# Performance work log

Hardware: AMD Instinct MI355X
Metric: run time of the kernel (lower is better)

The kernel has to match this reference:

```python
import jax, jax.numpy as jnp
import numpy as np

B, T, E, H = 2, 2048, 1024, 16
D = E // H            # head dim = 64
ROT = D // 2          # rotary_dim = 32 (only first half of head dim is rotated)
THETA = 10000.0


def _rope(x):
    # x: (B, H, T, D). Faithful to rotary_embedding_torch.rotate_queries_or_keys
    # with dim=ROT: rotate first ROT features, interleaved-pair style, pass rest.
    t = x.shape[-2]
    inv = 1.0 / (THETA ** (jnp.arange(0, ROT, 2, dtype=jnp.float32) / ROT))   # (ROT//2,)
    freqs = jnp.arange(t, dtype=jnp.float32)[:, None] * inv[None, :]          # (T, ROT//2)
    freqs = jnp.repeat(freqs, 2, axis=-1)                                      # (T, ROT)
    cos, sin = jnp.cos(freqs), jnp.sin(freqs)
    xr, xp = x[..., :ROT], x[..., ROT:]
    p = xr.reshape(*xr.shape[:-1], ROT // 2, 2)
    rot = jnp.stack((-p[..., 1], p[..., 0]), axis=-1).reshape(xr.shape)
    return jnp.concatenate([xr * cos + rot * sin, xp], axis=-1)


def setup_inputs() -> dict:
    key = jax.random.key(0)
    k1, k2, k3 = jax.random.split(key, 3)
    query = jax.random.normal(k1, (B, T, E), dtype=jnp.float32)
    inputs = {
        "query": query,
        "key": query,            # ignored (cross_attention=False)
        "value": query,          # ignored
        "padding_mask": jnp.ones((B, T), dtype=bool),
        "in_proj_weight": jax.random.uniform(k2, (3 * E, E), dtype=jnp.float32),
        "out_proj_weight": jax.random.normal(k3, (E, E), dtype=jnp.float32) * (E ** -0.5),
    }
    return inputs


def reference(query, key, value, padding_mask, in_proj_weight, out_proj_weight):
    # cross_attention=False: key/value are overwritten by query
    key = query
    value = query
    q = query @ in_proj_weight[:E].T
    k = key @ in_proj_weight[E:2 * E].T
    v = value @ in_proj_weight[2 * E:].T
    # NOTE: raw reshape (B,T,E)->(B,H,T,D), exactly as in the torch module
    q = q.reshape(B, H, T, D)
    k = k.reshape(B, H, T, D)
    v = v.reshape(B, H, T, D)
    q = _rope(q)
    k = _rope(k)   # causal self-attention path: rotate keys too
    causal = jnp.tril(jnp.ones((T, T), dtype=bool))                 # (T, T)
    mask = causal[None, None] & padding_mask[:, None, None, :]      # (B,1,T,T) -> broadcast over H
    scores = jnp.einsum("bhqd,bhkd->bhqk", q, k) / jnp.sqrt(jnp.float32(D))
    scores = jnp.where(mask, scores, -jnp.inf)
    attn = jax.nn.softmax(scores, axis=-1)
    x = jnp.einsum("bhqk,bhkd->bhqd", attn, v)
    x = x.reshape(B, T, E)      # raw reshape back, as in torch
    return x @ out_proj_weight.T
```

## Files before the change

### kernel.cpp

```cpp
#include <hip/hip_runtime.h>
#include <stdint.h>

#define T_ 2048
#define E_ 1024

typedef __attribute__((ext_vector_type(8))) __bf16 bf16x8;
typedef __attribute__((ext_vector_type(4))) float f32x4;

__device__ __forceinline__ void gload_lds16(const void* g, void* l) {
  __builtin_amdgcn_global_load_lds(
      (const __attribute__((address_space(1))) unsigned int*)g,
      (__attribute__((address_space(3))) unsigned int*)l, 16, 0, 0);
}

__global__ __launch_bounds__(256) void k_split(const float4* __restrict__ src,
                                               ushort4* __restrict__ hi,
                                               ushort4* __restrict__ lo, int n4) {
  int i = blockIdx.x * 256 + threadIdx.x;
  if (i >= n4) return;
  float4 x = src[i];
  float xs[4] = {x.x, x.y, x.z, x.w};
  union { __bf16 b[4]; ushort4 u; } H, L;
#pragma unroll
  for (int j = 0; j < 4; ++j) {
    __bf16 h = (__bf16)xs[j];
    H.b[j] = h;
    L.b[j] = (__bf16)(xs[j] - (float)h);
  }
  hi[i] = H.u;
  lo[i] = L.u;
}

__global__ __launch_bounds__(256) void k_cvt(const float4* __restrict__ src,
                                             ushort4* __restrict__ dst, int n4) {
  int i = blockIdx.x * 256 + threadIdx.x;
  if (i >= n4) return;
  float4 x = src[i];
  float xs[4] = {x.x, x.y, x.z, x.w};
  union { __bf16 b[4]; ushort4 u; } H;
#pragma unroll
  for (int j = 0; j < 4; ++j) H.b[j] = (__bf16)xs[j];
  dst[i] = H.u;
}

__global__ __launch_bounds__(256) void k_table(float2* __restrict__ cs) {
  int i = blockIdx.x * 256 + threadIdx.x;
  int t = i >> 4, f = i & 15;
  double inv = pow(10000.0, -(double)f / 16.0);
  double ang = (double)t * inv;
  cs[i] = make_float2((float)cos(ang), (float)sin(ang));
}

template <int EPI, bool HILO>
__global__ __launch_bounds__(256) void k_gemm(const __bf16* __restrict__ Ah,
                                              const __bf16* __restrict__ Al,
                                              const __bf16* __restrict__ Bh,
                                              const __bf16* __restrict__ Bl,
                                              int M, int N, int K,
                                              const float2* __restrict__ cs,
                                              __bf16* __restrict__ qhi,
                                              __bf16* __restrict__ qlo,
                                              __bf16* __restrict__ khi,
                                              __bf16* __restrict__ klo,
                                              __bf16* __restrict__ v16,
                                              float* __restrict__ C32) {
  __shared__ __align__(16) __bf16 AsH[128 * 32];
  __shared__ __align__(16) __bf16 BsH[128 * 32];
  __shared__ __align__(16) __bf16 AsL[HILO ? 128 * 32 : 4];
  __shared__ __align__(16) __bf16 BsL[HILO ? 128 * 32 : 4];
  const int tid = threadIdx.x, lane = tid & 63, w = tid >> 6;
  const int wm = w >> 1, wn = w & 1;
  const int g = lane >> 4, d = lane & 15;
  const int m0 = blockIdx.y * 128, n0 = blockIdx.x * 128;

  f32x4 acc[4][4];
#pragma unroll
  for (int i = 0; i < 4; ++i)
#pragma unroll
    for (int j = 0; j < 4; ++j) acc[i][j] = (f32x4)(0.0f);

  const int row0 = tid >> 2, kc = tid & 3;
  const int row1 = 64 + row0;

  for (int k0 = 0; k0 < K; k0 += 32) {
    __syncthreads();
    gload_lds16(Ah + (size_t)(m0 + row0) * K + k0 + kc * 8, &AsH[w * 512]);
    gload_lds16(Ah + (size_t)(m0 + row1) * K + k0 + kc * 8, &AsH[2048 + w * 512]);
    gload_lds16(Bh + (size_t)(n0 + row0) * K + k0 + kc * 8, &BsH[w * 512]);
    gload_lds16(Bh + (size_t)(n0 + row1) * K + k0 + kc * 8, &BsH[2048 + w * 512]);
    if constexpr (HILO) {
      gload_lds16(Al + (size_t)(m0 + row0) * K + k0 + kc * 8, &AsL[w * 512]);
      gload_lds16(Al + (size_t)(m0 + row1) * K + k0 + kc * 8, &AsL[2048 + w * 512]);
      gload_lds16(Bl + (size_t)(n0 + row0) * K + k0 + kc * 8, &BsL[w * 512]);
      gload_lds16(Bl + (size_t)(n0 + row1) * K + k0 + kc * 8, &BsL[2048 + w * 512]);
    }
    __syncthreads();
    bf16x8 ah[4], bh[4], al[4], bl[4];
#pragma unroll
    for (int i = 0; i < 4; ++i) {
      ah[i] = *(const bf16x8*)&AsH[(wm * 64 + i * 16 + d) * 32 + g * 8];
      bh[i] = *(const bf16x8*)&BsH[(wn * 64 + i * 16 + d) * 32 + g * 8];
      if constexpr (HILO) {
        al[i] = *(const bf16x8*)&AsL[(wm * 64 + i * 16 + d) * 32 + g * 8];
        bl[i] = *(const bf16x8*)&BsL[(wn * 64 + i * 16 + d) * 32 + g * 8];
      }
    }
#pragma unroll
    for (int i = 0; i < 4; ++i)
#pragma unroll
      for (int j = 0; j < 4; ++j) {
        acc[i][j] = __builtin_amdgcn_mfma_f32_16x16x32_bf16(ah[i], bh[j], acc[i][j], 0, 0, 0);
        if constexpr (HILO) {
          acc[i][j] = __builtin_amdgcn_mfma_f32_16x16x32_bf16(al[i], bh[j], acc[i][j], 0, 0, 0);
          acc[i][j] = __builtin_amdgcn_mfma_f32_16x16x32_bf16(ah[i], bl[j], acc[i][j], 0, 0, 0);
        }
      }
  }

#pragma unroll
  for (int i = 0; i < 4; ++i) {
    const int rbase = m0 + wm * 64 + i * 16 + g * 4;
#pragma unroll
    for (int j = 0; j < 4; ++j) {
      const int col = n0 + wn * 64 + j * 16 + d;
#pragma unroll
      for (int r = 0; r < 4; ++r) {
        const float vv = acc[i][j][r];
        const int row = rbase + r;
        if constexpr (EPI == 0) {
          const float xp = __shfl_xor(vv, 1);
          const int which = col >> 10;
          const int cl = col & 1023;
          const int d2 = cl & 63;
          const int t2 = (row & 127) * 16 + (cl >> 6);
          float y;
          if (d2 < 32) {
            const float2 cse = cs[t2 * 16 + (d2 >> 1)];
            y = (d2 & 1) ? (vv * cse.x + xp * cse.y) : (vv * cse.x - xp * cse.y);
          } else {
            y = vv;
          }
          if (which == 0) y *= 0.18033688011112042f;
          const __bf16 hi = (__bf16)y;
          const __bf16 lo = (__bf16)(y - (float)hi);
          const size_t off = (size_t)row * 1024 + cl;
          (which ? khi : qhi)[off] = hi;
          (which ? klo : qlo)[off] = lo;
        } else if constexpr (EPI == 1) {
          C32[(size_t)row * N + col] = vv;
        } else {
          v16[(size_t)row * N + col] = (__bf16)vv;
        }
      }
    }
  }
}

__global__ __launch_bounds__(256) void k_vtrans(const __bf16* __restrict__ v16,
                                                __bf16* __restrict__ v16t) {
  __shared__ __bf16 TB[64][72];
  const int p = blockIdx.y, t0 = blockIdx.x * 64;
  const int tid = threadIdx.x;
  const int r = tid >> 2, c4 = (tid & 3) * 16;
  const __bf16* src = v16 + ((size_t)p * 2048 + t0 + r) * 64 + c4;
  bf16x8 A = *(const bf16x8*)src;
  bf16x8 B2 = *(const bf16x8*)(src + 8);
#pragma unroll
  for (int e = 0; e < 8; ++e) {
    TB[c4 + e][r] = A[e];
    TB[c4 + 8 + e][r] = B2[e];
  }
  __syncthreads();
  const int dd = tid >> 2, cc = (tid & 3) * 16;
  __bf16* dst = v16t + ((size_t)p * 64 + dd) * 2048 + t0 + cc;
  *(bf16x8*)dst = *(const bf16x8*)&TB[dd][cc];
  *(bf16x8*)(dst + 8) = *(const bf16x8*)&TB[dd][cc + 8];
}

__global__ __launch_bounds__(512, 4) void k_attn(const __bf16* __restrict__ qhi,
                                                 const __bf16* __restrict__ qlo,
                                                 const __bf16* __restrict__ khi,
                                                 const __bf16* __restrict__ klo,
                                                 const __bf16* __restrict__ v16t,
                                                 __bf16* __restrict__ x16,
                                                 float* __restrict__ po,
                                                 float* __restrict__ pm,
                                                 float* __restrict__ pl_) {
  __shared__ __align__(16) __bf16 KH[2][64 * 64];
  __shared__ __align__(16) __bf16 KL[2][64 * 64];
  __shared__ __align__(16) __bf16 VT[2][64 * 64];
  __shared__ __align__(16) __bf16 PL[8][16 * 72];

  const int x = blockIdx.x, panel = blockIdx.y;
  int qt, c, nc;
  if (x < 16)      { qt = 7 - (x >> 2);        c = x & 3;        nc = 4; }
  else if (x < 20) { qt = 3 - ((x - 16) >> 1); c = (x - 16) & 1; nc = 2; }
  else             { qt = 21 - x;              c = 0;            nc = 1; }
  const int sg = x;
  const int q0 = qt * 256;
  const int jmax = 4 * qt + 3;

  const int tid = threadIdx.x, lane = tid & 63, w = tid >> 6;
  const int g = lane >> 4, d = lane & 15;
  const size_t hb = (size_t)panel * T_ * 64;

  bf16x8 qh[2][2], ql[2][2];
#pragma unroll
  for (int rb = 0; rb < 2; ++rb) {
    const int rbi = w * 2 + rb;
    const size_t qrow = hb + (size_t)(q0 + rbi * 16 + d) * 64;
    qh[rb][0] = *(const bf16x8*)&qhi[qrow + g * 8];
    qh[rb][1] = *(const bf16x8*)&qhi[qrow + 32 + g * 8];
    ql[rb][0] = *(const bf16x8*)&qlo[qrow + g * 8];
    ql[rb][1] = *(const bf16x8*)&qlo[qrow + 32 + g * 8];
  }

  f32x4 o[2][4];
#pragma unroll
  for (int rb = 0; rb < 2; ++rb)
#pragma unroll
    for (int i = 0; i < 4; ++i) o[rb][i] = (f32x4)(0.0f);
  float m_[2] = {-__builtin_inff(), -__builtin_inff()};
  float l_[2] = {0.0f, 0.0f};

  const int kr = tid >> 3, kc = tid & 7;
  const int swz = (kc ^ (kr & 7)) * 8;
  const __bf16* kB = khi + hb;
  const __bf16* lB = klo + hb;
  const __bf16* vB = v16t + (size_t)panel * (64 * T_);

#define STAGE(j, b)                                                        \
  {                                                                        \
    gload_lds16(kB + (size_t)((j) * 64 + kr) * 64 + swz, &KH[b][w * 512]); \
    gload_lds16(lB + (size_t)((j) * 64 + kr) * 64 + swz, &KL[b][w * 512]); \
    gload_lds16(vB + (size_t)kr * T_ + (j) * 64 + swz, &VT[b][w * 512]);   \
  }

  STAGE(c, 0);
  int cur = 0;
  for (int j = c; j <= jmax; j += nc) {
    __syncthreads();
    const int jn = j + nc;
    if (jn <= jmax) STAGE(jn, cur ^ 1);

#pragma unroll
    for (int rb = 0; rb < 2; ++rb) {
      const int rbi = w * 2 + rb;
      const int qrow0 = q0 + rbi * 16;
      if (j * 64 > qrow0 + 15) continue;

      f32x4 s[4];
      __builtin_amdgcn_s_setprio(1);
#pragma unroll
      for (int f = 0; f < 4; ++f) {
        f32x4 accs = (f32x4)(0.0f);
        const int colr = f * 16 + d;
#pragma unroll
        for (int ds = 0; ds < 2; ++ds) {
          const int slot = ((ds * 4 + g) ^ (colr & 7)) * 8;
          const bf16x8 kf = *(const bf16x8*)&KH[cur][colr * 64 + slot];
          const bf16x8 lf = *(const bf16x8*)&KL[cur][colr * 64 + slot];
          accs = __builtin_amdgcn_mfma_f32_16x16x32_bf16(kf, qh[rb][ds], accs, 0, 0, 0);
          accs = __builtin_amdgcn_mfma_f32_16x16x32_bf16(kf, ql[rb][ds], accs, 0, 0, 0);
          accs = __builtin_amdgcn_mfma_f32_16x16x32_bf16(lf, qh[rb][ds], accs, 0, 0, 0);
        }
        s[f] = accs;
      }
      __builtin_amdgcn_s_setprio(0);

      if (j * 64 + 63 > qrow0) {
        const int qq = qrow0 + d;
#pragma unroll
        for (int f = 0; f < 4; ++f)
#pragma unroll
          for (int r = 0; r < 4; ++r) {
            const int kv = j * 64 + f * 16 + g * 4 + r;
            if (kv > qq) s[f][r] = -30000.0f;
          }
      }

      float pmax = fmaxf(fmaxf(s[0][0], s[0][1]), fmaxf(s[0][2], s[0][3]));
#pragma unroll
      for (int f = 1; f < 4; ++f)
        pmax = fmaxf(pmax, fmaxf(fmaxf(s[f][0], s[f][1]), fmaxf(s[f][2], s[f][3])));
      pmax = fmaxf(pmax, __shfl_xor(pmax, 16));
      pmax = fmaxf(pmax, __shfl_xor(pmax, 32));

      if (!__all(pmax - m_[rb] <= 11.5f)) {
        const float mnew = fmaxf(m_[rb], pmax);
        const float fac = exp2f(m_[rb] - mnew);
        m_[rb] = mnew;
        float facr[4];
#pragma unroll
        for (int r = 0; r < 4; ++r)
          facr[r] = __shfl(fac, (lane & 48) | (g * 4 + r));
#pragma unroll
        for (int ni = 0; ni < 4; ++ni)
#pragma unroll
          for (int r = 0; r < 4; ++r) o[rb][ni][r] *= facr[r];
        l_[rb] *= fac;
      }

      float sum = 0.0f;
#pragma unroll
      for (int f = 0; f < 4; ++f) {
        union { __bf16 b[4]; ushort4 u4; } pk;
#pragma unroll
        for (int r = 0; r < 4; ++r) {
          const float pv = exp2f(s[f][r] - m_[rb]);
          sum += pv;
          pk.b[r] = (__bf16)pv;
        }
        *(ushort4*)&PL[w][d * 72 + f * 16 + g * 4] = pk.u4;
      }
      sum += __shfl_xor(sum, 16);
      sum += __shfl_xor(sum, 32);
      l_[rb] += sum;

      __builtin_amdgcn_s_setprio(1);
#pragma unroll
      for (int ks = 0; ks < 2; ++ks) {
        const bf16x8 pa = *(const bf16x8*)&PL[w][d * 72 + ks * 32 + g * 8];
#pragma unroll
        for (int ni = 0; ni < 4; ++ni) {
          const bf16x8 vf =
              *(const bf16x8*)&VT[cur][(ni * 16 + d) * 64 + (((ks * 4 + g) ^ (d & 7)) * 8)];
          o[rb][ni] = __builtin_amdgcn_mfma_f32_16x16x32_bf16(pa, vf, o[rb][ni], 0, 0, 0);
        }
      }
      __builtin_amdgcn_s_setprio(0);
    }
    cur ^= 1;
  }

  if (nc == 1) {
#pragma unroll
    for (int rb = 0; rb < 2; ++rb) {
      const int rbi = w * 2 + rb;
      float lr[4];
#pragma unroll
      for (int r = 0; r < 4; ++r)
        lr[r] = __shfl(l_[rb], (lane & 48) | (g * 4 + r));
#pragma unroll
      for (int ni = 0; ni < 4; ++ni)
#pragma unroll
        for (int r = 0; r < 4; ++r) {
          const size_t row = hb + (size_t)(q0 + rbi * 16 + g * 4 + r) * 64;
          x16[row + ni * 16 + d] = (__bf16)(o[rb][ni][r] / lr[r]);
        }
    }
  } else {
    const int slot = panel * 20 + sg;
#pragma unroll
    for (int rb = 0; rb < 2; ++rb) {
      const int rbi = w * 2 + rb;
#pragma unroll
      for (int ni = 0; ni < 4; ++ni)
#pragma unroll
        for (int r = 0; r < 4; ++r) {
          const int rowin = rbi * 16 + g * 4 + r;
          po[(size_t)slot * 16384 + rowin * 64 + ni * 16 + d] = o[rb][ni][r];
        }
      if (g == 0) {
        pm[slot * 256 + rbi * 16 + d] = m_[rb];
        pl_[slot * 256 + rbi * 16 + d] = l_[rb];
      }
    }
  }
#undef STAGE
}

__global__ __launch_bounds__(256) void k_combine(const float* __restrict__ po,
                                                 const float* __restrict__ pm,
                                                 const float* __restrict__ pl_,
                                                 __bf16* __restrict__ x16) {
  const int p = blockIdx.y;
  const int li = blockIdx.x * 256 + threadIdx.x;
  const int d = li & 63;
  const int t2 = 512 + (li >> 6);
  const int qt = t2 >> 8;
  const int rowin = t2 & 255;
  const int nc = (qt >= 4) ? 4 : 2;
  const int base = (qt >= 4) ? (7 - qt) * 4 : 16 + (3 - qt) * 2;
  const int s0 = p * 20 + base;
  float M = -__builtin_inff();
  for (int s = 0; s < nc; ++s) M = fmaxf(M, pm[(s0 + s) * 256 + rowin]);
  float L = 0.0f, O = 0.0f;
  for (int s = 0; s < nc; ++s) {
    const float ww = exp2f(pm[(s0 + s) * 256 + rowin] - M);
    L += pl_[(s0 + s) * 256 + rowin] * ww;
    O += po[(size_t)(s0 + s) * 16384 + rowin * 64 + d] * ww;
  }
  x16[((size_t)p * T_ + t2) * 64 + d] = (__bf16)(O / L);
}

extern "C" void kernel_launch(void* const* d_in, const int* in_sizes, int n_in,
                              void* d_out, int out_size, void* d_ws, size_t ws_size,
                              hipStream_t stream) {
  const float* query = (const float*)d_in[0];
  const float* win = (const float*)d_in[4];
  const float* wout = (const float*)d_in[5];
  float* out = (float*)d_out;

  const size_t MB = 1024 * 1024;
  char* ws = (char*)d_ws;
  __bf16* xh = (__bf16*)(ws);
  __bf16* xl = (__bf16*)(ws + 8 * MB);
  __bf16* whh = (__bf16*)(ws + 16 * MB);
  __bf16* whl = (__bf16*)(ws + 22 * MB);
  __bf16* wob = (__bf16*)(ws + 28 * MB);
  float* pm = (float*)(ws + 30 * MB);
  float* pl_ = (float*)(ws + 30 * MB + 656 * 1024);
  float* po = (float*)(ws + 32 * MB);
  __bf16* qhi = (__bf16*)(ws + 72 * MB);
  __bf16* qlo = (__bf16*)(ws + 80 * MB);
  __bf16* khi = (__bf16*)(ws + 88 * MB);
  __bf16* klo = (__bf16*)(ws + 96 * MB);
  __bf16* x16 = (__bf16*)(ws + 104 * MB);
  float2* cs = (float2*)(ws + 112 * MB);
  __bf16* v16 = (__bf16*)(ws + 64 * MB);
  __bf16* v16t = (__bf16*)(ws);

  k_split<<<4096, 256, 0, stream>>>((const float4*)query, (ushort4*)xh, (ushort4*)xl,
                                    4096 * 1024 / 4);
  k_split<<<3072, 256, 0, stream>>>((const float4*)win, (ushort4*)whh, (ushort4*)whl,
                                    3072 * 1024 / 4);
  k_cvt<<<1024, 256, 0, stream>>>((const float4*)wout, (ushort4*)wob, 1024 * 1024 / 4);
  k_table<<<128, 256, 0, stream>>>(cs);

  dim3 gqk(16, 32);
  k_gemm<0, true><<<gqk, 256, 0, stream>>>(xh, xl, whh, whl, 4096, 2048, 1024, cs,
                                           qhi, qlo, khi, klo, nullptr, nullptr);
  dim3 gv(8, 32);
  k_gemm<2, false><<<gv, 256, 0, stream>>>(xh, nullptr, whh + (size_t)2048 * 1024, nullptr,
                                           4096, 1024, 1024, nullptr, nullptr, nullptr,
                                           nullptr, nullptr, v16, nullptr);

  dim3 gt(32, 32);
  k_vtrans<<<gt, 256, 0, stream>>>(v16, v16t);

  dim3 ga(22, 32);
  k_attn<<<ga, 512, 0, stream>>>(qhi, qlo, khi, klo, v16t, x16, po, pm, pl_);

  dim3 gc(384, 32);
  k_combine<<<gc, 256, 0, stream>>>(po, pm, pl_, x16);

  dim3 go(8, 32);
  k_gemm<1, false><<<go, 256, 0, stream>>>(x16, nullptr, wob, nullptr, 4096, 1024, 1024,
                                           nullptr, nullptr, nullptr, nullptr, nullptr,
                                           nullptr, out);
}
```

Measured before the change: 227.2 us.

## Halve attention KV tile to 32 and raise occupancy to six blocks per CU

Splits each 64-key tile into two 32-key sub-tiles with double-buffered LDS, shrinking shared memory per block and re-swizzling the K/V/P layouts. Low-precision Q fragments are reloaded from global per sub-tile instead of held in registers. Launch bounds move from 4 to 6 blocks per CU. The aim is higher occupancy to hide latency, at the cost of twice as many barriers, smaller MFMA batches per sync, and repeated global Q-lo loads.

```diff
diff --git a/kernel.cpp b/kernel.cpp
--- a/kernel.cpp
+++ b/kernel.cpp
@@ -177,7 +177,7 @@
   *(bf16x8*)(dst + 8) = *(const bf16x8*)&TB[dd][cc + 8];
 }
 
-__global__ __launch_bounds__(512, 4) void k_attn(const __bf16* __restrict__ qhi,
+__global__ __launch_bounds__(512, 6) void k_attn(const __bf16* __restrict__ qhi,
                                                  const __bf16* __restrict__ qlo,
                                                  const __bf16* __restrict__ khi,
                                                  const __bf16* __restrict__ klo,
@@ -186,10 +186,10 @@
                                                  float* __restrict__ po,
                                                  float* __restrict__ pm,
                                                  float* __restrict__ pl_) {
-  __shared__ __align__(16) __bf16 KH[2][64 * 64];
-  __shared__ __align__(16) __bf16 KL[2][64 * 64];
-  __shared__ __align__(16) __bf16 VT[2][64 * 64];
-  __shared__ __align__(16) __bf16 PL[8][16 * 72];
+  __shared__ __align__(16) __bf16 KH[2][32 * 64];
+  __shared__ __align__(16) __bf16 KL[2][32 * 64];
+  __shared__ __align__(16) __bf16 VT[2][64 * 32];
+  __shared__ __align__(16) __bf16 PL[8][16 * 32];
 
   const int x = blockIdx.x, panel = blockIdx.y;
   int qt, c, nc;
@@ -204,15 +204,13 @@
   const int g = lane >> 4, d = lane & 15;
   const size_t hb = (size_t)panel * T_ * 64;
 
-  bf16x8 qh[2][2], ql[2][2];
+  bf16x8 qh[2][2];
 #pragma unroll
   for (int rb = 0; rb < 2; ++rb) {
     const int rbi = w * 2 + rb;
     const size_t qrow = hb + (size_t)(q0 + rbi * 16 + d) * 64;
     qh[rb][0] = *(const bf16x8*)&qhi[qrow + g * 8];
     qh[rb][1] = *(const bf16x8*)&qhi[qrow + 32 + g * 8];
-    ql[rb][0] = *(const bf16x8*)&qlo[qrow + g * 8];
-    ql[rb][1] = *(const bf16x8*)&qlo[qrow + 32 + g * 8];
   }
 
   f32x4 o[2][4];
@@ -223,114 +221,131 @@
   float m_[2] = {-__builtin_inff(), -__builtin_inff()};
   float l_[2] = {0.0f, 0.0f};
 
-  const int kr = tid >> 3, kc = tid & 7;
-  const int swz = (kc ^ (kr & 7)) * 8;
   const __bf16* kB = khi + hb;
   const __bf16* lB = klo + hb;
   const __bf16* vB = v16t + (size_t)panel * (64 * T_);
-
-#define STAGE(j, b)                                                        \
-  {                                                                        \
-    gload_lds16(kB + (size_t)((j) * 64 + kr) * 64 + swz, &KH[b][w * 512]); \
-    gload_lds16(lB + (size_t)((j) * 64 + kr) * 64 + swz, &KL[b][w * 512]); \
-    gload_lds16(vB + (size_t)kr * T_ + (j) * 64 + swz, &VT[b][w * 512]);   \
-  }
-
-  STAGE(c, 0);
+  const int dsw = (d >> 1) & 3;
+
+#define STAGE(tt, b)                                                              \
+  {                                                                               \
+    if (w < 4) {                                                                  \
+      const int r_ = w * 8 + (lane >> 3);                                         \
+      const int cg_ = ((lane & 7) ^ (r_ & 7)) * 8;                                \
+      gload_lds16(kB + (size_t)((tt) * 32 + r_) * 64 + cg_, &KH[b][w * 512]);     \
+      const int dv_ = w * 16 + (lane >> 2);                                       \
+      const int vg_ = ((lane & 3) ^ ((dv_ >> 1) & 3)) * 8;                        \
+      gload_lds16(vB + (size_t)dv_ * T_ + (tt) * 32 + vg_, &VT[b][w * 512]);      \
+    } else {                                                                      \
+      const int r_ = (w - 4) * 8 + (lane >> 3);                                   \
+      const int cg_ = ((lane & 7) ^ (r_ & 7)) * 8;                                \
+      gload_lds16(lB + (size_t)((tt) * 32 + r_) * 64 + cg_, &KL[b][(w - 4) * 512]); \
+    }                                                                             \
+  }
+
+  STAGE(2 * c, 0);
   int cur = 0;
-  for (int j = c; j <= jmax; j += nc) {
-    __syncthreads();
-    const int jn = j + nc;
-    if (jn <= jmax) STAGE(jn, cur ^ 1);
-
-#pragma unroll
-    for (int rb = 0; rb < 2; ++rb) {
-      const int rbi = w * 2 + rb;
-      const int qrow0 = q0 + rbi * 16;
-      if (j * 64 > qrow0 + 15) continue;
-
-      f32x4 s[4];
-      __builtin_amdgcn_s_setprio(1);
-#pragma unroll
-      for (int f = 0; f < 4; ++f) {
-        f32x4 accs = (f32x4)(0.0f);
-        const int colr = f * 16 + d;
-#pragma unroll
-        for (int ds = 0; ds < 2; ++ds) {
-          const int slot = ((ds * 4 + g) ^ (colr & 7)) * 8;
-          const bf16x8 kf = *(const bf16x8*)&KH[cur][colr * 64 + slot];
-          const bf16x8 lf = *(const bf16x8*)&KL[cur][colr * 64 + slot];
-          accs = __builtin_amdgcn_mfma_f32_16x16x32_bf16(kf, qh[rb][ds], accs, 0, 0, 0);
-          accs = __builtin_amdgcn_mfma_f32_16x16x32_bf16(kf, ql[rb][ds], accs, 0, 0, 0);
-          accs = __builtin_amdgcn_mfma_f32_16x16x32_bf16(lf, qh[rb][ds], accs, 0, 0, 0);
-        }
-        s[f] = accs;
-      }
-      __builtin_amdgcn_s_setprio(0);
-
-      if (j * 64 + 63 > qrow0) {
-        const int qq = qrow0 + d;
-#pragma unroll
-        for (int f = 0; f < 4; ++f)
+  for (int jj = c; jj <= jmax; jj += nc) {
+#pragma unroll
+    for (int h = 0; h < 2; ++h) {
+      const int t = 2 * jj + h;
+      __syncthreads();
+      if (h == 0) {
+        STAGE(t + 1, cur ^ 1);
+      } else {
+        const int jn = jj + nc;
+        if (jn <= jmax) STAGE(2 * jn, cur ^ 1);
+      }
+
+#pragma unroll
+      for (int rb = 0; rb < 2; ++rb) {
+        const int rbi = w * 2 + rb;
+        const int qrow0 = q0 + rbi * 16;
+        if (t * 32 > qrow0 + 15) continue;
+
+        const size_t qrow = hb + (size_t)(qrow0 + d) * 64;
+        const bf16x8 ql0 = *(const bf16x8*)&qlo[qrow + g * 8];
+        const bf16x8 ql1 = *(const bf16x8*)&qlo[qrow + 32 + g * 8];
+
+        f32x4 s[2];
+        __builtin_amdgcn_s_setprio(1);
+#pragma unroll
+        for (int f = 0; f < 2; ++f) {
+          f32x4 accs = (f32x4)(0.0f);
+          const int colr = f * 16 + d;
+#pragma unroll
+          for (int ds = 0; ds < 2; ++ds) {
+            const int slot = ((ds * 4 + g) ^ (colr & 7)) * 8;
+            const bf16x8 kf = *(const bf16x8*)&KH[cur][colr * 64 + slot];
+            const bf16x8 lf = *(const bf16x8*)&KL[cur][colr * 64 + slot];
+            const bf16x8 qv = (ds == 0) ? ql0 : ql1;
+            accs = __builtin_amdgcn_mfma_f32_16x16x32_bf16(kf, qh[rb][ds], accs, 0, 0, 0);
+            accs = __builtin_amdgcn_mfma_f32_16x16x32_bf16(kf, qv, accs, 0, 0, 0);
+            accs = __builtin_amdgcn_mfma_f32_16x16x32_bf16(lf, qh[rb][ds], accs, 0, 0, 0);
+          }
+          s[f] = accs;
+        }
+        __builtin_amdgcn_s_setprio(0);
+
+        if (t * 32 + 31 > qrow0) {
+          const int qq = qrow0 + d;
+#pragma unroll
+          for (int f = 0; f < 2; ++f)
+#pragma unroll
+            for (int r = 0; r < 4; ++r) {
+              const int kv = t * 32 + f * 16 + g * 4 + r;
+              if (kv > qq) s[f][r] = -30000.0f;
+            }
+        }
+
+        float pmax = fmaxf(fmaxf(s[0][0], s[0][1]), fmaxf(s[0][2], s[0][3]));
+        pmax = fmaxf(pmax, fmaxf(fmaxf(s[1][0], s[1][1]), fmaxf(s[1][2], s[1][3])));
+        pmax = fmaxf(pmax, __shfl_xor(pmax, 16));
+        pmax = fmaxf(pmax, __shfl_xor(pmax, 32));
+
+        if (!__all(pmax - m_[rb] <= 11.5f)) {
+          const float mnew = fmaxf(m_[rb], pmax);
+          const float fac = exp2f(m_[rb] - mnew);
+          m_[rb] = mnew;
+          float facr[4];
+#pragma unroll
+          for (int r = 0; r < 4; ++r)
+            facr[r] = __shfl(fac, (lane & 48) | (g * 4 + r));
+#pragma unroll
+          for (int ni = 0; ni < 4; ++ni)
+#pragma unroll
+            for (int r = 0; r < 4; ++r) o[rb][ni][r] *= facr[r];
+          l_[rb] *= fac;
+        }
+
+        float sum = 0.0f;
+#pragma unroll
+        for (int f = 0; f < 2; ++f) {
+          union { __bf16 b[4]; ushort4 u4; } pk;
 #pragma unroll
           for (int r = 0; r < 4; ++r) {
-            const int kv = j * 64 + f * 16 + g * 4 + r;
-            if (kv > qq) s[f][r] = -30000.0f;
+            const float pv = exp2f(s[f][r] - m_[rb]);
+            sum += pv;
+            pk.b[r] = (__bf16)pv;
           }
-      }
-
-      float pmax = fmaxf(fmaxf(s[0][0], s[0][1]), fmaxf(s[0][2], s[0][3]));
-#pragma unroll
-      for (int f = 1; f < 4; ++f)
-        pmax = fmaxf(pmax, fmaxf(fmaxf(s[f][0], s[f][1]), fmaxf(s[f][2], s[f][3])));
-      pmax = fmaxf(pmax, __shfl_xor(pmax, 16));
-      pmax = fmaxf(pmax, __shfl_xor(pmax, 32));
-
-      if (!__all(pmax - m_[rb] <= 11.5f)) {
-        const float mnew = fmaxf(m_[rb], pmax);
-        const float fac = exp2f(m_[rb] - mnew);
-        m_[rb] = mnew;
-        float facr[4];
-#pragma unroll
-        for (int r = 0; r < 4; ++r)
-          facr[r] = __shfl(fac, (lane & 48) | (g * 4 + r));
-#pragma unroll
-        for (int ni = 0; ni < 4; ++ni)
-#pragma unroll
-          for (int r = 0; r < 4; ++r) o[rb][ni][r] *= facr[r];
-        l_[rb] *= fac;
-      }
-
-      float sum = 0.0f;
-#pragma unroll
-      for (int f = 0; f < 4; ++f) {
-        union { __bf16 b[4]; ushort4 u4; } pk;
-#pragma unroll
-        for (int r = 0; r < 4; ++r) {
-          const float pv = exp2f(s[f][r] - m_[rb]);
-          sum += pv;
-          pk.b[r] = (__bf16)pv;
-        }
-        *(ushort4*)&PL[w][d * 72 + f * 16 + g * 4] = pk.u4;
-      }
-      sum += __shfl_xor(sum, 16);
-      sum += __shfl_xor(sum, 32);
-      l_[rb] += sum;
-
-      __builtin_amdgcn_s_setprio(1);
-#pragma unroll
-      for (int ks = 0; ks < 2; ++ks) {
-        const bf16x8 pa = *(const bf16x8*)&PL[w][d * 72 + ks * 32 + g * 8];
+          const int gsl = ((f * 2 + (g >> 1)) ^ dsw) * 8 + (g & 1) * 4;
+          *(ushort4*)&PL[w][d * 32 + gsl] = pk.u4;
+        }
+        sum += __shfl_xor(sum, 16);
+        sum += __shfl_xor(sum, 32);
+        l_[rb] += sum;
+
+        __builtin_amdgcn_s_setprio(1);
+        const int vsl = (g ^ dsw) * 8;
+        const bf16x8 pa = *(const bf16x8*)&PL[w][d * 32 + vsl];
 #pragma unroll
         for (int ni = 0; ni < 4; ++ni) {
-          const bf16x8 vf =
-              *(const bf16x8*)&VT[cur][(ni * 16 + d) * 64 + (((ks * 4 + g) ^ (d & 7)) * 8)];
+          const bf16x8 vf = *(const bf16x8*)&VT[cur][(ni * 16 + d) * 32 + vsl];
           o[rb][ni] = __builtin_amdgcn_mfma_f32_16x16x32_bf16(pa, vf, o[rb][ni], 0, 0, 0);
         }
-      }
-      __builtin_amdgcn_s_setprio(0);
-    }
-    cur ^= 1;
+        __builtin_amdgcn_s_setprio(0);
+      }
+      cur ^= 1;
+    }
   }
 
   if (nc == 1) {
```

New measurement: 370.9 us. 1.63x slower.

## Balance causal attention work with fixed nine-tile chunks per block

Applied to the files above, without the earlier changes.

Replaces the per-query-tile split-KV schedule (22 blocks per panel, uneven split counts) with 16 blocks per panel, each handling exactly nine consecutive KV tiles from a flattened causal work list. A block may span two query tiles, writing partial results for each. Every query row now goes through the combine kernel, which recomputes slot ranges from the flattened layout. The aim is even per-block work and a shorter tail, at the cost of more partial-result traffic, a larger combine pass and extra query reloads at segment boundaries. The workspace layout is reshuffled so x16 aliases the qhi region.

```diff
diff --git a/kernel.cpp b/kernel.cpp
--- a/kernel.cpp
+++ b/kernel.cpp
@@ -191,37 +191,20 @@
   __shared__ __align__(16) __bf16 VT[2][64 * 64];
   __shared__ __align__(16) __bf16 PL[8][16 * 72];
 
-  const int x = blockIdx.x, panel = blockIdx.y;
-  int qt, c, nc;
-  if (x < 16)      { qt = 7 - (x >> 2);        c = x & 3;        nc = 4; }
-  else if (x < 20) { qt = 3 - ((x - 16) >> 1); c = (x - 16) & 1; nc = 2; }
-  else             { qt = 21 - x;              c = 0;            nc = 1; }
-  const int sg = x;
-  const int q0 = qt * 256;
-  const int jmax = 4 * qt + 3;
+  const int b = blockIdx.x, panel = blockIdx.y;
+  const int u0 = 9 * b;
+  int qtA = 0;
+  while (2 * (qtA + 1) * (qtA + 2) <= u0) ++qtA;
+  const int cumA = 2 * qtA * (qtA + 1);
+  const int cumB = 2 * (qtA + 1) * (qtA + 2);
+  const int jloA = u0 - cumA;
+  const bool two = (u0 + 9 > cumB);
+  const int jhiA = two ? (cumB - 1 - cumA) : (u0 + 8 - cumA);
+  const int jhiB = u0 + 8 - cumB;
 
   const int tid = threadIdx.x, lane = tid & 63, w = tid >> 6;
   const int g = lane >> 4, d = lane & 15;
   const size_t hb = (size_t)panel * T_ * 64;
-
-  bf16x8 qh[2][2], ql[2][2];
-#pragma unroll
-  for (int rb = 0; rb < 2; ++rb) {
-    const int rbi = w * 2 + rb;
-    const size_t qrow = hb + (size_t)(q0 + rbi * 16 + d) * 64;
-    qh[rb][0] = *(const bf16x8*)&qhi[qrow + g * 8];
-    qh[rb][1] = *(const bf16x8*)&qhi[qrow + 32 + g * 8];
-    ql[rb][0] = *(const bf16x8*)&qlo[qrow + g * 8];
-    ql[rb][1] = *(const bf16x8*)&qlo[qrow + 32 + g * 8];
-  }
-
-  f32x4 o[2][4];
-#pragma unroll
-  for (int rb = 0; rb < 2; ++rb)
-#pragma unroll
-    for (int i = 0; i < 4; ++i) o[rb][i] = (f32x4)(0.0f);
-  float m_[2] = {-__builtin_inff(), -__builtin_inff()};
-  float l_[2] = {0.0f, 0.0f};
 
   const int kr = tid >> 3, kc = tid & 7;
   const int swz = (kc ^ (kr & 7)) * 8;
@@ -229,128 +212,141 @@
   const __bf16* lB = klo + hb;
   const __bf16* vB = v16t + (size_t)panel * (64 * T_);
 
-#define STAGE(j, b)                                                        \
-  {                                                                        \
-    gload_lds16(kB + (size_t)((j) * 64 + kr) * 64 + swz, &KH[b][w * 512]); \
-    gload_lds16(lB + (size_t)((j) * 64 + kr) * 64 + swz, &KL[b][w * 512]); \
-    gload_lds16(vB + (size_t)kr * T_ + (j) * 64 + swz, &VT[b][w * 512]);   \
-  }
-
-  STAGE(c, 0);
+#define STAGE(j, bb)                                                        \
+  {                                                                         \
+    gload_lds16(kB + (size_t)((j) * 64 + kr) * 64 + swz, &KH[bb][w * 512]); \
+    gload_lds16(lB + (size_t)((j) * 64 + kr) * 64 + swz, &KL[bb][w * 512]); \
+    gload_lds16(vB + (size_t)kr * T_ + (j) * 64 + swz, &VT[bb][w * 512]);   \
+  }
+
   int cur = 0;
-  for (int j = c; j <= jmax; j += nc) {
-    __syncthreads();
-    const int jn = j + nc;
-    if (jn <= jmax) STAGE(jn, cur ^ 1);
-
+  STAGE(jloA, 0);
+
+  for (int seg = 0; seg < 2; ++seg) {
+    if (seg && !two) break;
+    const int qt = qtA + seg;
+    const int jlo = seg ? 0 : jloA;
+    const int jhi = seg ? jhiB : jhiA;
+    const int q0 = qt << 8;
+
+    bf16x8 qh[2][2], ql[2][2];
 #pragma unroll
     for (int rb = 0; rb < 2; ++rb) {
       const int rbi = w * 2 + rb;
-      const int qrow0 = q0 + rbi * 16;
-      if (j * 64 > qrow0 + 15) continue;
-
-      f32x4 s[4];
-      __builtin_amdgcn_s_setprio(1);
-#pragma unroll
-      for (int f = 0; f < 4; ++f) {
-        f32x4 accs = (f32x4)(0.0f);
-        const int colr = f * 16 + d;
-#pragma unroll
-        for (int ds = 0; ds < 2; ++ds) {
-          const int slot = ((ds * 4 + g) ^ (colr & 7)) * 8;
-          const bf16x8 kf = *(const bf16x8*)&KH[cur][colr * 64 + slot];
-          const bf16x8 lf = *(const bf16x8*)&KL[cur][colr * 64 + slot];
-          accs = __builtin_amdgcn_mfma_f32_16x16x32_bf16(kf, qh[rb][ds], accs, 0, 0, 0);
-          accs = __builtin_amdgcn_mfma_f32_16x16x32_bf16(kf, ql[rb][ds], accs, 0, 0, 0);
-          accs = __builtin_amdgcn_mfma_f32_16x16x32_bf16(lf, qh[rb][ds], accs, 0, 0, 0);
-        }
-        s[f] = accs;
-      }
-      __builtin_amdgcn_s_setprio(0);
-
-      if (j * 64 + 63 > qrow0) {
-        const int qq = qrow0 + d;
-#pragma unroll
-        for (int f = 0; f < 4; ++f)
+      const size_t qrow = hb + (size_t)(q0 + rbi * 16 + d) * 64;
+      qh[rb][0] = *(const bf16x8*)&qhi[qrow + g * 8];
+      qh[rb][1] = *(const bf16x8*)&qhi[qrow + 32 + g * 8];
+      ql[rb][0] = *(const bf16x8*)&qlo[qrow + g * 8];
+      ql[rb][1] = *(const bf16x8*)&qlo[qrow + 32 + g * 8];
+    }
+
+    f32x4 o[2][4];
+#pragma unroll
+    for (int rb = 0; rb < 2; ++rb)
+#pragma unroll
+      for (int i = 0; i < 4; ++i) o[rb][i] = (f32x4)(0.0f);
+    float m_[2] = {-__builtin_inff(), -__builtin_inff()};
+    float l_[2] = {0.0f, 0.0f};
+
+    for (int j = jlo; j <= jhi; ++j) {
+      __syncthreads();
+      if (j < jhi) {
+        STAGE(j + 1, cur ^ 1);
+      } else if (!seg && two) {
+        STAGE(0, cur ^ 1);
+      }
+
+#pragma unroll
+      for (int rb = 0; rb < 2; ++rb) {
+        const int rbi = w * 2 + rb;
+        const int qrow0 = q0 + rbi * 16;
+        if (j * 64 > qrow0 + 15) continue;
+
+        f32x4 s[4];
+        __builtin_amdgcn_s_setprio(1);
+#pragma unroll
+        for (int f = 0; f < 4; ++f) {
+          f32x4 accs = (f32x4)(0.0f);
+          const int colr = f * 16 + d;
+#pragma unroll
+          for (int ds = 0; ds < 2; ++ds) {
+            const int slot = ((ds * 4 + g) ^ (colr & 7)) * 8;
+            const bf16x8 kf = *(const bf16x8*)&KH[cur][colr * 64 + slot];
+            const bf16x8 lf = *(const bf16x8*)&KL[cur][colr * 64 + slot];
+            accs = __builtin_amdgcn_mfma_f32_16x16x32_bf16(kf, qh[rb][ds], accs, 0, 0, 0);
+            accs = __builtin_amdgcn_mfma_f32_16x16x32_bf16(kf, ql[rb][ds], accs, 0, 0, 0);
+            accs = __builtin_amdgcn_mfma_f32_16x16x32_bf16(lf, qh[rb][ds], accs, 0, 0, 0);
+          }
+          s[f] = accs;
+        }
+        __builtin_amdgcn_s_setprio(0);
+
+        if (j * 64 + 63 > qrow0) {
+          const int qq = qrow0 + d;
+#pragma unroll
+          for (int f = 0; f < 4; ++f)
+#pragma unroll
+            for (int r = 0; r < 4; ++r) {
+              const int kv = j * 64 + f * 16 + g * 4 + r;
+              if (kv > qq) s[f][r] = -30000.0f;
+            }
+        }
+
+        float pmax = fmaxf(fmaxf(s[0][0], s[0][1]), fmaxf(s[0][2], s[0][3]));
+#pragma unroll
+        for (int f = 1; f < 4; ++f)
+          pmax = fmaxf(pmax, fmaxf(fmaxf(s[f][0], s[f][1]), fmaxf(s[f][2], s[f][3])));
+        pmax = fmaxf(pmax, __shfl_xor(pmax, 16));
+        pmax = fmaxf(pmax, __shfl_xor(pmax, 32));
+
+        if (!__all(pmax - m_[rb] <= 11.5f)) {
+          const float mnew = fmaxf(m_[rb], pmax);
+          const float fac = exp2f(m_[rb] - mnew);
+          m_[rb] = mnew;
+          float facr[4];
+#pragma unroll
+          for (int r = 0; r < 4; ++r)
+            facr[r] = __shfl(fac, (lane & 48) | (g * 4 + r));
+#pragma unroll
+          for (int ni = 0; ni < 4; ++ni)
+#pragma unroll
+            for (int r = 0; r < 4; ++r) o[rb][ni][r] *= facr[r];
+          l_[rb] *= fac;
+        }
+
+        float sum = 0.0f;
+#pragma unroll
+        for (int f = 0; f < 4; ++f) {
+          union { __bf16 b[4]; ushort4 u4; } pk;
 #pragma unroll
           for (int r = 0; r < 4; ++r) {
-            const int kv = j * 64 + f * 16 + g * 4 + r;
-            if (kv > qq) s[f][r] = -30000.0f;
+            const float pv = exp2f(s[f][r] - m_[rb]);
+            sum += pv;
+            pk.b[r] = (__bf16)pv;
           }
-      }
-
-      float pmax = fmaxf(fmaxf(s[0][0], s[0][1]), fmaxf(s[0][2], s[0][3]));
-#pragma unroll
-      for (int f = 1; f < 4; ++f)
-        pmax = fmaxf(pmax, fmaxf(fmaxf(s[f][0], s[f][1]), fmaxf(s[f][2], s[f][3])));
-      pmax = fmaxf(pmax, __shfl_xor(pmax, 16));
-      pmax = fmaxf(pmax, __shfl_xor(pmax, 32));
-
-      if (!__all(pmax - m_[rb] <= 11.5f)) {
-        const float mnew = fmaxf(m_[rb], pmax);
-        const float fac = exp2f(m_[rb] - mnew);
-        m_[rb] = mnew;
-        float facr[4];
-#pragma unroll
-        for (int r = 0; r < 4; ++r)
-          facr[r] = __shfl(fac, (lane & 48) | (g * 4 + r));
-#pragma unroll
-        for (int ni = 0; ni < 4; ++ni)
-#pragma unroll
-          for (int r = 0; r < 4; ++r) o[rb][ni][r] *= facr[r];
-        l_[rb] *= fac;
-      }
-
-      float sum = 0.0f;
-#pragma unroll
-      for (int f = 0; f < 4; ++f) {
-        union { __bf16 b[4]; ushort4 u4; } pk;
-#pragma unroll
-        for (int r = 0; r < 4; ++r) {
-          const float pv = exp2f(s[f][r] - m_[rb]);
-          sum += pv;
-          pk.b[r] = (__bf16)pv;
-        }
-        *(ushort4*)&PL[w][d * 72 + f * 16 + g * 4] = pk.u4;
-      }
-      sum += __shfl_xor(sum, 16);
-      sum += __shfl_xor(sum, 32);
-      l_[rb] += sum;
-
-      __builtin_amdgcn_s_setprio(1);
-#pragma unroll
-      for (int ks = 0; ks < 2; ++ks) {
-        const bf16x8 pa = *(const bf16x8*)&PL[w][d * 72 + ks * 32 + g * 8];
-#pragma unroll
-        for (int ni = 0; ni < 4; ++ni) {
-          const bf16x8 vf =
-              *(const bf16x8*)&VT[cur][(ni * 16 + d) * 64 + (((ks * 4 + g) ^ (d & 7)) * 8)];
-          o[rb][ni] = __builtin_amdgcn_mfma_f32_16x16x32_bf16(pa, vf, o[rb][ni], 0, 0, 0);
-        }
-      }
-      __builtin_amdgcn_s_setprio(0);
-    }
-    cur ^= 1;
-  }
-
-  if (nc == 1) {
-#pragma unroll
-    for (int rb = 0; rb < 2; ++rb) {
-      const int rbi = w * 2 + rb;
-      float lr[4];
-#pragma unroll
-      for (int r = 0; r < 4; ++r)
-        lr[r] = __shfl(l_[rb], (lane & 48) | (g * 4 + r));
-#pragma unroll
-      for (int ni = 0; ni < 4; ++ni)
-#pragma unroll
-        for (int r = 0; r < 4; ++r) {
-          const size_t row = hb + (size_t)(q0 + rbi * 16 + g * 4 + r) * 64;
-          x16[row + ni * 16 + d] = (__bf16)(o[rb][ni][r] / lr[r]);
-        }
-    }
-  } else {
-    const int slot = panel * 20 + sg;
+          *(ushort4*)&PL[w][d * 72 + f * 16 + g * 4] = pk.u4;
+        }
+        sum += __shfl_xor(sum, 16);
+        sum += __shfl_xor(sum, 32);
+        l_[rb] += sum;
+
+        __builtin_amdgcn_s_setprio(1);
+#pragma unroll
+        for (int ks = 0; ks < 2; ++ks) {
+          const bf16x8 pa = *(const bf16x8*)&PL[w][d * 72 + ks * 32 + g * 8];
+#pragma unroll
+          for (int ni = 0; ni < 4; ++ni) {
+            const bf16x8 vf =
+                *(const bf16x8*)&VT[cur][(ni * 16 + d) * 64 + (((ks * 4 + g) ^ (d & 7)) * 8)];
+            o[rb][ni] = __builtin_amdgcn_mfma_f32_16x16x32_bf16(pa, vf, o[rb][ni], 0, 0, 0);
+          }
+        }
+        __builtin_amdgcn_s_setprio(0);
+      }
+      cur ^= 1;
+    }
+
+    const int slot = panel * 23 + b + qt;
 #pragma unroll
     for (int rb = 0; rb < 2; ++rb) {
       const int rbi = w * 2 + rb;
@@ -377,12 +373,12 @@
   const int p = blockIdx.y;
   const int li = blockIdx.x * 256 + threadIdx.x;
   const int d = li & 63;
-  const int t2 = 512 + (li >> 6);
+  const int t2 = li >> 6;
   const int qt = t2 >> 8;
   const int rowin = t2 & 255;
-  const int nc = (qt >= 4) ? 4 : 2;
-  const int base = (qt >= 4) ? (7 - qt) * 4 : 16 + (3 - qt) * 2;
-  const int s0 = p * 20 + base;
+  const int cq = 2 * qt * (qt + 1);
+  const int nc = (cq + 4 * qt + 3) / 9 - cq / 9 + 1;
+  const int s0 = p * 23 + cq / 9 + qt;
   float M = -__builtin_inff();
   for (int s = 0; s < nc; ++s) M = fmaxf(M, pm[(s0 + s) * 256 + rowin]);
   float L = 0.0f, O = 0.0f;
@@ -403,6 +399,7 @@
   float* out = (float*)d_out;
 
   const size_t MB = 1024 * 1024;
+  const size_t KB = 1024;
   char* ws = (char*)d_ws;
   __bf16* xh = (__bf16*)(ws);
   __bf16* xl = (__bf16*)(ws + 8 * MB);
@@ -410,14 +407,14 @@
   __bf16* whl = (__bf16*)(ws + 22 * MB);
   __bf16* wob = (__bf16*)(ws + 28 * MB);
   float* pm = (float*)(ws + 30 * MB);
-  float* pl_ = (float*)(ws + 30 * MB + 656 * 1024);
+  float* pl_ = (float*)(ws + 30 * MB + 768 * KB);
+  float2* cs = (float2*)(ws + 31 * MB + 512 * KB);
   float* po = (float*)(ws + 32 * MB);
-  __bf16* qhi = (__bf16*)(ws + 72 * MB);
-  __bf16* qlo = (__bf16*)(ws + 80 * MB);
-  __bf16* khi = (__bf16*)(ws + 88 * MB);
-  __bf16* klo = (__bf16*)(ws + 96 * MB);
-  __bf16* x16 = (__bf16*)(ws + 104 * MB);
-  float2* cs = (float2*)(ws + 112 * MB);
+  __bf16* qhi = (__bf16*)(ws + 78 * MB);
+  __bf16* qlo = (__bf16*)(ws + 86 * MB);
+  __bf16* khi = (__bf16*)(ws + 94 * MB);
+  __bf16* klo = (__bf16*)(ws + 102 * MB);
+  __bf16* x16 = (__bf16*)(ws + 78 * MB);
   __bf16* v16 = (__bf16*)(ws + 64 * MB);
   __bf16* v16t = (__bf16*)(ws);
 
@@ -439,10 +436,10 @@
   dim3 gt(32, 32);
   k_vtrans<<<gt, 256, 0, stream>>>(v16, v16t);
 
-  dim3 ga(22, 32);
+  dim3 ga(16, 32);
   k_attn<<<ga, 512, 0, stream>>>(qhi, qlo, khi, klo, v16t, x16, po, pm, pl_);
 
-  dim3 gc(384, 32);
+  dim3 gc(512, 32);
   k_combine<<<gc, 256, 0, stream>>>(po, pm, pl_, x16);
 
   dim3 go(8, 32);
```

Measured after the change: 217.0 us. -4.5%, faster.
